# Optimization experiments

Hardware: AMD Instinct MI355X
Metric: run time of the kernel (lower is better)

## Reference

```python
import jax, jax.numpy as jnp
import numpy as np

EPS = 1e-5

def _bn_relu(x, gamma, beta):
    # BatchNorm1d in training mode: batch statistics over the point dim, biased var
    m = jnp.mean(x, axis=0)
    v = jnp.var(x, axis=0)
    y = (x - m) * jax.lax.rsqrt(v + EPS) * gamma + beta
    return jax.nn.relu(y)

def setup_inputs() -> dict:
    key = jax.random.key(0)
    ks = jax.random.split(key, 8)
    N_in, N_out = 65536, 262144
    C_in, C_skip, C_out = 512, 256, 256
    return {
        "feat": jax.random.normal(ks[0], (N_in, C_in), jnp.float32),
        "skip_feat": jax.random.normal(ks[1], (N_out, C_skip), jnp.float32),
        "cluster": jax.random.randint(ks[2], (N_out,), 0, N_in, jnp.int32),
        "W_proj": jax.random.normal(ks[3], (C_in, C_out), jnp.float32) / np.sqrt(C_in),
        "b_proj": jax.random.normal(ks[4], (C_out,), jnp.float32) * 0.02,
        "gamma_p": jnp.ones((C_out,), jnp.float32),
        "beta_p": jnp.zeros((C_out,), jnp.float32),
        "W_skip": jax.random.normal(ks[5], (C_skip, C_out), jnp.float32) / np.sqrt(C_skip),
        "b_skip": jax.random.normal(ks[6], (C_out,), jnp.float32) * 0.02,
        "gamma_s": jnp.ones((C_out,), jnp.float32),
        "beta_s": jnp.zeros((C_out,), jnp.float32),
    }

def reference(feat, skip_feat, cluster, W_proj, b_proj, gamma_p, beta_p,
              W_skip, b_skip, gamma_s, beta_s):
    # proj branch on coarse points, then unpool via gather
    h = _bn_relu(feat @ W_proj + b_proj, gamma_p, beta_p)      # [N_in, C_out]
    h = h[cluster]                                             # [N_out, C_out]
    # skip branch on fine points
    s = _bn_relu(skip_feat @ W_skip + b_skip, gamma_s, beta_s) # [N_out, C_out]
    return h + s
```

## Files before the change

### kernel.cpp

```cpp
#include <hip/hip_runtime.h>
#include <hip/hip_bf16.h>
#include <stdint.h>
#include <stddef.h>

typedef __attribute__((ext_vector_type(8))) short bf16x8;
typedef __attribute__((ext_vector_type(4))) short bf16x4;
typedef __attribute__((ext_vector_type(4))) float f32x4;

__device__ __forceinline__ unsigned short f2bf(float x) {
    union { float f; unsigned u; } v; v.f = x;
    unsigned r = v.u + 0x7fffu + ((v.u >> 16) & 1u);
    return (unsigned short)(r >> 16);
}
__device__ __forceinline__ float bf2f(unsigned short h) {
    union { unsigned u; float f; } v; v.u = ((unsigned)h) << 16;
    return v.f;
}

extern "C" __global__ void prep_w_kernel(const float* __restrict__ Wp, const float* __restrict__ Ws,
                                         unsigned short* __restrict__ WpT, unsigned short* __restrict__ WsT,
                                         int Cin, int Cs, int Cout)
{
    int tid = blockIdx.x * blockDim.x + threadIdx.x;
    int np = Cin * Cout;
    int ns = Cs * Cout;
    if (tid < np) {
        int k = tid / Cout, n = tid - k * Cout;
        WpT[n * Cin + k] = f2bf(Wp[tid]);
    } else if (tid < np + ns) {
        int t = tid - np;
        int k = t / Cout, n = t - k * Cout;
        WsT[n * Cs + k] = f2bf(Ws[t]);
    }
}

extern "C" __global__ __launch_bounds__(256, 2)
void gemm_bn_kernel(const float* __restrict__ A, const unsigned short* __restrict__ WT,
                    const float* __restrict__ bias,
                    unsigned short* __restrict__ outb,
                    float* __restrict__ gsum, float* __restrict__ gsumsq,
                    int M, int K, int N)
{
    const int m0 = blockIdx.x * 128;
    const int n0 = blockIdx.y * 128;
    const int tid = threadIdx.x;
    const int lane = tid & 63;
    const int wave = tid >> 6;
    const int wm = (wave >> 1) << 6;
    const int wn = (wave & 1) << 6;
    const int q = lane >> 4;
    const int l15 = lane & 15;

    __shared__ unsigned short sA[128 * 40];
    __shared__ unsigned short sB[128 * 40];

    f32x4 acc[4][4];
#pragma unroll
    for (int i = 0; i < 4; ++i)
#pragma unroll
        for (int j = 0; j < 4; ++j)
            acc[i][j] = (f32x4){0.f, 0.f, 0.f, 0.f};

    const int a_m = tid >> 3;
    const int a_f = tid & 7;
    const int b_n = tid >> 2;
    const int b_seg = tid & 3;

    const float* Abase = A + (size_t)(m0 + a_m) * K + a_f * 4;
    const unsigned short* Bbase = WT + (size_t)(n0 + b_n) * K + b_seg * 8;

    const int ksteps = K >> 5;
    for (int kt = 0; kt < ksteps; ++kt) {
        const int k0 = kt << 5;
        __syncthreads();
#pragma unroll
        for (int r = 0; r < 4; ++r) {
            f32x4 av = *(const f32x4*)(Abase + (size_t)(32 * r) * K + k0);
            bf16x4 pk;
            pk[0] = (short)f2bf(av[0]); pk[1] = (short)f2bf(av[1]);
            pk[2] = (short)f2bf(av[2]); pk[3] = (short)f2bf(av[3]);
            *(bf16x4*)(&sA[(a_m + 32 * r) * 40 + a_f * 4]) = pk;
        }
#pragma unroll
        for (int r = 0; r < 2; ++r) {
            bf16x8 wv = *(const bf16x8*)(Bbase + (size_t)(64 * r) * K + k0);
            *(bf16x8*)(&sB[(b_n + 64 * r) * 40 + b_seg * 8]) = wv;
        }
        __syncthreads();

        bf16x8 afr[4], bfr[4];
#pragma unroll
        for (int mi = 0; mi < 4; ++mi)
            afr[mi] = *(const bf16x8*)(&sA[(wm + mi * 16 + l15) * 40 + q * 8]);
#pragma unroll
        for (int ni = 0; ni < 4; ++ni)
            bfr[ni] = *(const bf16x8*)(&sB[(wn + ni * 16 + l15) * 40 + q * 8]);
#pragma unroll
        for (int mi = 0; mi < 4; ++mi)
#pragma unroll
            for (int ni = 0; ni < 4; ++ni)
                acc[mi][ni] = __builtin_amdgcn_mfma_f32_16x16x32_bf16(afr[mi], bfr[ni], acc[mi][ni], 0, 0, 0);
    }

#pragma unroll
    for (int ni = 0; ni < 4; ++ni) {
        const int c = n0 + wn + ni * 16 + l15;
        const float bv = bias[c];
        float s1 = 0.f, s2 = 0.f;
#pragma unroll
        for (int mi = 0; mi < 4; ++mi) {
            const int row = m0 + wm + mi * 16 + (q << 2);
#pragma unroll
            for (int r = 0; r < 4; ++r) {
                float v = acc[mi][ni][r] + bv;
                s1 += v; s2 += v * v;
                outb[(size_t)(row + r) * N + c] = f2bf(v);
            }
        }
        s1 += __shfl_xor(s1, 16); s2 += __shfl_xor(s2, 16);
        s1 += __shfl_xor(s1, 32); s2 += __shfl_xor(s2, 32);
        if (q == 0) {
            atomicAdd(&gsum[c], s1);
            atomicAdd(&gsumsq[c], s2);
        }
    }
}

extern "C" __global__ void finalize_kernel(const float* __restrict__ stats,
                                           const float* __restrict__ gamma_p, const float* __restrict__ beta_p,
                                           const float* __restrict__ gamma_s, const float* __restrict__ beta_s,
                                           float* __restrict__ ab, float invNp, float invNs, int Cout)
{
    int c = threadIdx.x;
    if (c < Cout) {
        float m = stats[c] * invNp;
        float var = stats[Cout + c] * invNp - m * m;
        float a = gamma_p[c] * rsqrtf(var + 1e-5f);
        ab[c] = a;
        ab[Cout + c] = beta_p[c] - m * a;
        float m2 = stats[2 * Cout + c] * invNs;
        float var2 = stats[3 * Cout + c] * invNs - m2 * m2;
        float a2 = gamma_s[c] * rsqrtf(var2 + 1e-5f);
        ab[2 * Cout + c] = a2;
        ab[3 * Cout + c] = beta_s[c] - m2 * a2;
    }
}

extern "C" __global__ __launch_bounds__(256)
void fuse_kernel(const unsigned short* __restrict__ hb, const unsigned short* __restrict__ sb,
                 const int* __restrict__ cluster, const float* __restrict__ ab,
                 float* __restrict__ out, int Cout)
{
    int idx = blockIdx.x * 256 + threadIdx.x;
    int i = idx >> 6;
    int c4 = (idx & 63) << 2;
    int j = cluster[i];
    bf16x4 h4 = *(const bf16x4*)(hb + (size_t)j * Cout + c4);
    bf16x4 s4 = *(const bf16x4*)(sb + (size_t)i * Cout + c4);
    f32x4 ap = *(const f32x4*)(ab + c4);
    f32x4 bp = *(const f32x4*)(ab + Cout + c4);
    f32x4 as = *(const f32x4*)(ab + 2 * Cout + c4);
    f32x4 bs = *(const f32x4*)(ab + 3 * Cout + c4);
    f32x4 o;
#pragma unroll
    for (int e = 0; e < 4; ++e) {
        float hv = bf2f((unsigned short)h4[e]) * ap[e] + bp[e];
        float sv = bf2f((unsigned short)s4[e]) * as[e] + bs[e];
        o[e] = fmaxf(hv, 0.f) + fmaxf(sv, 0.f);
    }
    *(f32x4*)(out + (size_t)i * Cout + c4) = o;
}

extern "C" void kernel_launch(void* const* d_in, const int* in_sizes, int n_in,
                              void* d_out, int out_size, void* d_ws, size_t ws_size,
                              hipStream_t stream)
{
    const float* feat    = (const float*)d_in[0];
    const float* skipf   = (const float*)d_in[1];
    const int*   cluster = (const int*)d_in[2];
    const float* W_proj  = (const float*)d_in[3];
    const float* b_proj  = (const float*)d_in[4];
    const float* gamma_p = (const float*)d_in[5];
    const float* beta_p  = (const float*)d_in[6];
    const float* W_skip  = (const float*)d_in[7];
    const float* b_skip  = (const float*)d_in[8];
    const float* gamma_s = (const float*)d_in[9];
    const float* beta_s  = (const float*)d_in[10];
    float* out = (float*)d_out;

    const int Cout = in_sizes[4];
    const int Cin  = in_sizes[3] / Cout;
    const int Cs   = in_sizes[7] / Cout;
    const int Nout = in_sizes[2];
    const int Nin  = in_sizes[0] / Cin;

    char* ws = (char*)d_ws;
    unsigned short* h_pre = (unsigned short*)ws; ws += (size_t)Nin * Cout * 2;
    unsigned short* s_pre = (unsigned short*)ws; ws += (size_t)Nout * Cout * 2;
    unsigned short* WpT   = (unsigned short*)ws; ws += (size_t)Cout * Cin * 2;
    unsigned short* WsT   = (unsigned short*)ws; ws += (size_t)Cout * Cs * 2;
    float* stats          = (float*)ws;          ws += (size_t)4 * Cout * 4;
    float* ab             = (float*)ws;

    hipMemsetAsync(stats, 0, 4 * Cout * sizeof(float), stream);

    int prep_total = Cin * Cout + Cs * Cout;
    prep_w_kernel<<<(prep_total + 255) / 256, 256, 0, stream>>>(W_proj, W_skip, WpT, WsT, Cin, Cs, Cout);

    dim3 g1(Nin / 128, Cout / 128);
    gemm_bn_kernel<<<g1, 256, 0, stream>>>(feat, WpT, b_proj, h_pre,
                                           stats, stats + Cout, Nin, Cin, Cout);

    dim3 g2(Nout / 128, Cout / 128);
    gemm_bn_kernel<<<g2, 256, 0, stream>>>(skipf, WsT, b_skip, s_pre,
                                           stats + 2 * Cout, stats + 3 * Cout, Nout, Cs, Cout);

    finalize_kernel<<<1, Cout, 0, stream>>>(stats, gamma_p, beta_p, gamma_s, beta_s,
                                            ab, 1.0f / (float)Nin, 1.0f / (float)Nout, Cout);

    size_t total_threads = (size_t)Nout * (Cout / 4);
    fuse_kernel<<<(unsigned)(total_threads / 256), 256, 0, stream>>>(h_pre, s_pre, cluster, ab, out, Cout);
}
```

Before: 820.9 us.

## Prefetch GEMM tiles in registers, transpose MFMA output, replace atomics with partial reduction

The GEMM loads the next k-tile's global data into registers while MFMAs run on the current tile. It swaps MFMA operands so each lane holds four consecutive channels, which allows vectorized bf16 stores. Per-column BN statistics are reduced in shared memory and written as per-block partials into the output buffer, then summed by a new reduce kernel instead of many global atomics. The grid is also reordered so the N tiles of one row block run next to each other, and the LDS padding is removed, which may add bank conflicts.

```diff
diff --git a/kernel.cpp b/kernel.cpp
--- a/kernel.cpp
+++ b/kernel.cpp
@@ -38,11 +38,11 @@
 void gemm_bn_kernel(const float* __restrict__ A, const unsigned short* __restrict__ WT,
                     const float* __restrict__ bias,
                     unsigned short* __restrict__ outb,
-                    float* __restrict__ gsum, float* __restrict__ gsumsq,
+                    float* __restrict__ Ppart,
                     int M, int K, int N)
 {
-    const int m0 = blockIdx.x * 128;
-    const int n0 = blockIdx.y * 128;
+    const int m0 = blockIdx.y * 128;
+    const int n0 = blockIdx.x * 128;
     const int tid = threadIdx.x;
     const int lane = tid & 63;
     const int wave = tid >> 6;
@@ -51,8 +51,8 @@
     const int q = lane >> 4;
     const int l15 = lane & 15;
 
-    __shared__ unsigned short sA[128 * 40];
-    __shared__ unsigned short sB[128 * 40];
+    __shared__ unsigned short sA[128 * 32];
+    __shared__ unsigned short sB[128 * 32];
 
     f32x4 acc[4][4];
 #pragma unroll
@@ -61,69 +61,120 @@
         for (int j = 0; j < 4; ++j)
             acc[i][j] = (f32x4){0.f, 0.f, 0.f, 0.f};
 
-    const int a_m = tid >> 3;
+    const int a_r = tid >> 3;
     const int a_f = tid & 7;
-    const int b_n = tid >> 2;
-    const int b_seg = tid & 3;
-
-    const float* Abase = A + (size_t)(m0 + a_m) * K + a_f * 4;
-    const unsigned short* Bbase = WT + (size_t)(n0 + b_n) * K + b_seg * 8;
+    const int b_r = tid >> 2;
+    const int b_s = tid & 3;
+
+    const float* Ap0 = A + (size_t)(m0 + a_r) * K + a_f * 4;
+    const unsigned short* Bp0 = WT + (size_t)(n0 + b_r) * K + b_s * 8;
 
     const int ksteps = K >> 5;
+
+    f32x4 ar[4];
+    bf16x8 br[2];
+#pragma unroll
+    for (int r = 0; r < 4; ++r) ar[r] = *(const f32x4*)(Ap0 + (size_t)(32 * r) * K);
+#pragma unroll
+    for (int r = 0; r < 2; ++r) br[r] = *(const bf16x8*)(Bp0 + (size_t)(64 * r) * K);
+
     for (int kt = 0; kt < ksteps; ++kt) {
-        const int k0 = kt << 5;
         __syncthreads();
 #pragma unroll
         for (int r = 0; r < 4; ++r) {
-            f32x4 av = *(const f32x4*)(Abase + (size_t)(32 * r) * K + k0);
             bf16x4 pk;
-            pk[0] = (short)f2bf(av[0]); pk[1] = (short)f2bf(av[1]);
-            pk[2] = (short)f2bf(av[2]); pk[3] = (short)f2bf(av[3]);
-            *(bf16x4*)(&sA[(a_m + 32 * r) * 40 + a_f * 4]) = pk;
-        }
-#pragma unroll
-        for (int r = 0; r < 2; ++r) {
-            bf16x8 wv = *(const bf16x8*)(Bbase + (size_t)(64 * r) * K + k0);
-            *(bf16x8*)(&sB[(b_n + 64 * r) * 40 + b_seg * 8]) = wv;
-        }
+            pk[0] = (short)f2bf(ar[r][0]); pk[1] = (short)f2bf(ar[r][1]);
+            pk[2] = (short)f2bf(ar[r][2]); pk[3] = (short)f2bf(ar[r][3]);
+            *(bf16x4*)(&sA[(a_r + 32 * r) * 32 + a_f * 4]) = pk;
+        }
+#pragma unroll
+        for (int r = 0; r < 2; ++r)
+            *(bf16x8*)(&sB[(b_r + 64 * r) * 32 + b_s * 8]) = br[r];
         __syncthreads();
 
+        if (kt + 1 < ksteps) {
+            const int k0n = (kt + 1) << 5;
+#pragma unroll
+            for (int r = 0; r < 4; ++r) ar[r] = *(const f32x4*)(Ap0 + (size_t)(32 * r) * K + k0n);
+#pragma unroll
+            for (int r = 0; r < 2; ++r) br[r] = *(const bf16x8*)(Bp0 + (size_t)(64 * r) * K + k0n);
+        }
+
         bf16x8 afr[4], bfr[4];
 #pragma unroll
         for (int mi = 0; mi < 4; ++mi)
-            afr[mi] = *(const bf16x8*)(&sA[(wm + mi * 16 + l15) * 40 + q * 8]);
+            afr[mi] = *(const bf16x8*)(&sA[(wm + mi * 16 + l15) * 32 + q * 8]);
 #pragma unroll
         for (int ni = 0; ni < 4; ++ni)
-            bfr[ni] = *(const bf16x8*)(&sB[(wn + ni * 16 + l15) * 40 + q * 8]);
+            bfr[ni] = *(const bf16x8*)(&sB[(wn + ni * 16 + l15) * 32 + q * 8]);
 #pragma unroll
         for (int mi = 0; mi < 4; ++mi)
 #pragma unroll
             for (int ni = 0; ni < 4; ++ni)
-                acc[mi][ni] = __builtin_amdgcn_mfma_f32_16x16x32_bf16(afr[mi], bfr[ni], acc[mi][ni], 0, 0, 0);
-    }
+                acc[mi][ni] = __builtin_amdgcn_mfma_f32_16x16x32_bf16(bfr[ni], afr[mi], acc[mi][ni], 0, 0, 0);
+    }
+
+    __syncthreads();
+    float* red = (float*)sA;
+    const int wmi = wave >> 1;
 
 #pragma unroll
     for (int ni = 0; ni < 4; ++ni) {
-        const int c = n0 + wn + ni * 16 + l15;
-        const float bv = bias[c];
-        float s1 = 0.f, s2 = 0.f;
+        const int chl = wn + ni * 16 + (q << 2);
+        const int nb = n0 + chl;
+        f32x4 bv = *(const f32x4*)(bias + nb);
+        f32x4 s1 = (f32x4){0.f, 0.f, 0.f, 0.f};
+        f32x4 s2 = (f32x4){0.f, 0.f, 0.f, 0.f};
 #pragma unroll
         for (int mi = 0; mi < 4; ++mi) {
-            const int row = m0 + wm + mi * 16 + (q << 2);
-#pragma unroll
-            for (int r = 0; r < 4; ++r) {
-                float v = acc[mi][ni][r] + bv;
-                s1 += v; s2 += v * v;
-                outb[(size_t)(row + r) * N + c] = f2bf(v);
-            }
-        }
-        s1 += __shfl_xor(s1, 16); s2 += __shfl_xor(s2, 16);
-        s1 += __shfl_xor(s1, 32); s2 += __shfl_xor(s2, 32);
-        if (q == 0) {
-            atomicAdd(&gsum[c], s1);
-            atomicAdd(&gsumsq[c], s2);
-        }
-    }
+            f32x4 v = acc[mi][ni] + bv;
+            s1 += v;
+            s2 += v * v;
+            bf16x4 pk;
+            pk[0] = (short)f2bf(v[0]); pk[1] = (short)f2bf(v[1]);
+            pk[2] = (short)f2bf(v[2]); pk[3] = (short)f2bf(v[3]);
+            *(bf16x4*)(&outb[(size_t)(m0 + wm + mi * 16 + l15) * N + nb]) = pk;
+        }
+#pragma unroll
+        for (int e = 0; e < 4; ++e) {
+            s1[e] += __shfl_xor(s1[e], 1); s2[e] += __shfl_xor(s2[e], 1);
+            s1[e] += __shfl_xor(s1[e], 2); s2[e] += __shfl_xor(s2[e], 2);
+            s1[e] += __shfl_xor(s1[e], 4); s2[e] += __shfl_xor(s2[e], 4);
+            s1[e] += __shfl_xor(s1[e], 8); s2[e] += __shfl_xor(s2[e], 8);
+        }
+        if (l15 == 0) {
+            *(f32x4*)(&red[(wmi * 2 + 0) * 128 + chl]) = s1;
+            *(f32x4*)(&red[(wmi * 2 + 1) * 128 + chl]) = s2;
+        }
+    }
+    __syncthreads();
+    {
+        const int arr = tid >> 7;
+        const int ch = tid & 127;
+        float v = red[arr * 128 + ch] + red[(2 + arr) * 128 + ch];
+        Ppart[((size_t)blockIdx.y * 2 + arr) * N + n0 + ch] = v;
+    }
+}
+
+extern "C" __global__ void reduce_kernel(const float* __restrict__ P1, const float* __restrict__ P2,
+                                         float* __restrict__ stats, int gx1, int gx2, int nb1, int Cout)
+{
+    const int b = blockIdx.x;
+    const int t = threadIdx.x;
+    const float* P;
+    int r0, rows, so;
+    if (b < nb1) { P = P1; r0 = b * 64;        rows = gx1 - r0; so = 0; }
+    else         { P = P2; r0 = (b - nb1) * 64; rows = gx2 - r0; so = 2 * Cout; }
+    if (rows > 64) rows = 64;
+    const int rw = 2 * Cout;
+    float a0 = 0.f, a1 = 0.f;
+    for (int r = 0; r < rows; ++r) {
+        const float* row = P + (size_t)(r0 + r) * rw;
+        a0 += row[t];
+        a1 += row[Cout + t];
+    }
+    atomicAdd(&stats[so + t], a0);
+    atomicAdd(&stats[so + Cout + t], a1);
 }
 
 extern "C" __global__ void finalize_kernel(const float* __restrict__ stats,
@@ -194,26 +245,34 @@
     const int Nout = in_sizes[2];
     const int Nin  = in_sizes[0] / Cin;
 
+    const int gx1 = Nin / 128;
+    const int gx2 = Nout / 128;
+
     char* ws = (char*)d_ws;
     unsigned short* h_pre = (unsigned short*)ws; ws += (size_t)Nin * Cout * 2;
     unsigned short* s_pre = (unsigned short*)ws; ws += (size_t)Nout * Cout * 2;
     unsigned short* WpT   = (unsigned short*)ws; ws += (size_t)Cout * Cin * 2;
     unsigned short* WsT   = (unsigned short*)ws; ws += (size_t)Cout * Cs * 2;
-    float* stats          = (float*)ws;          ws += (size_t)4 * Cout * 4;
     float* ab             = (float*)ws;
+
+    float* P1    = out;
+    float* P2    = P1 + (size_t)gx1 * 2 * Cout;
+    float* stats = P2 + (size_t)gx2 * 2 * Cout;
 
     hipMemsetAsync(stats, 0, 4 * Cout * sizeof(float), stream);
 
     int prep_total = Cin * Cout + Cs * Cout;
     prep_w_kernel<<<(prep_total + 255) / 256, 256, 0, stream>>>(W_proj, W_skip, WpT, WsT, Cin, Cs, Cout);
 
-    dim3 g1(Nin / 128, Cout / 128);
-    gemm_bn_kernel<<<g1, 256, 0, stream>>>(feat, WpT, b_proj, h_pre,
-                                           stats, stats + Cout, Nin, Cin, Cout);
-
-    dim3 g2(Nout / 128, Cout / 128);
-    gemm_bn_kernel<<<g2, 256, 0, stream>>>(skipf, WsT, b_skip, s_pre,
-                                           stats + 2 * Cout, stats + 3 * Cout, Nout, Cs, Cout);
+    dim3 g1(Cout / 128, gx1);
+    gemm_bn_kernel<<<g1, 256, 0, stream>>>(feat, WpT, b_proj, h_pre, P1, Nin, Cin, Cout);
+
+    dim3 g2(Cout / 128, gx2);
+    gemm_bn_kernel<<<g2, 256, 0, stream>>>(skipf, WsT, b_skip, s_pre, P2, Nout, Cs, Cout);
+
+    const int nb1 = (gx1 + 63) / 64;
+    const int nb2 = (gx2 + 63) / 64;
+    reduce_kernel<<<nb1 + nb2, 256, 0, stream>>>(P1, P2, stats, gx1, gx2, nb1, Cout);
 
     finalize_kernel<<<1, Cout, 0, stream>>>(stats, gamma_p, beta_p, gamma_s, beta_s,
                                             ab, 1.0f / (float)Nin, 1.0f / (float)Nout, Cout);
```

New measurement: 730.6 us. 11.0% less time.
